# Optimization experiments

Measured on AMD Instinct MI355X. Metric: run time of the kernel, lower is better.

Reference implementation:

```python
import jax, jax.numpy as jnp
import numpy as np

FWD_W = 1.0
BWD_W = 1.0
EPS = 1e-12  # guard sqrt gradient at exact zero


def setup_inputs() -> dict:
    key = jax.random.key(0)
    k1, k2 = jax.random.split(key)
    pred = jax.random.normal(k1, (4, 8192, 3), dtype=jnp.float32)
    target = jax.random.normal(k2, (4, 8192, 3), dtype=jnp.float32)
    return {"pred": pred, "target": target}


def reference(pred, target):
    # pairwise Euclidean distances (torch.cdist, p=2): (B, N, M)
    sq = (jnp.sum(pred * pred, axis=-1)[:, :, None]
          + jnp.sum(target * target, axis=-1)[:, None, :]
          - 2.0 * jnp.einsum('bnd,bmd->bnm', pred, target))
    dist = jnp.sqrt(jnp.maximum(sq, EPS))
    forward_dist = jnp.min(dist, axis=2)   # (B, N): pred -> nearest target
    backward_dist = jnp.min(dist, axis=1)  # (B, M): target -> nearest pred
    total = FWD_W * jnp.sum(forward_dist, axis=1) + BWD_W * jnp.sum(backward_dist, axis=1)
    return jnp.mean(total)  # reduction='mean'
```

## Files before the change

### kernel.cpp

```cpp
#include <hip/hip_runtime.h>
#include <math.h>

#define BATCH   4
#define NPTS    8192
#define THREADS 256
#define NQTOT   (2 * BATCH * NPTS)
#define TSPLIT  4
#define THALF   (NPTS / TSPLIT)

typedef _Float16 h8  __attribute__((ext_vector_type(8)));
typedef float    f16v __attribute__((ext_vector_type(16)));

__global__ __launch_bounds__(THREADS)
void chamfer_transform(const float* __restrict__ pred,
                       const float* __restrict__ target,
                       h8* __restrict__ trans_il)
{
    const int p   = blockIdx.x * THREADS + threadIdx.x;
    const int arr = p >> 15;
    const int pb  = p & 32767;

    const float* src = (arr ? target : pred) + (size_t)pb * 3;
    const float x = src[0], y = src[1], z = src[2];

    const _Float16 hx = (_Float16)x;  const float lxf = x - (float)hx;
    const _Float16 hy = (_Float16)y;  const float lyf = y - (float)hy;
    const _Float16 hz = (_Float16)z;  const float lzf = z - (float)hz;
    const _Float16 lx = (_Float16)lxf, ly = (_Float16)lyf, lz = (_Float16)lzf;

    const float tx = (float)hx + (float)lx;
    const float ty = (float)hy + (float)ly;
    const float tz = (float)hz + (float)lz;
    const float tt = fmaf(tx, tx, fmaf(ty, ty, tz * tz));
    const _Float16 tth = (_Float16)tt;
    const _Float16 ttl = (_Float16)(tt - (float)tth);

    const _Float16 n2 = (_Float16)(-2.0f);
    h8 lo = { n2 * hx, n2 * hy, n2 * hz, tth,
              n2 * hx, n2 * hy, n2 * hz, ttl };
    h8 hi = { n2 * lx, n2 * ly, n2 * lz, (_Float16)0.0f,
              (_Float16)0.0f, (_Float16)0.0f, (_Float16)0.0f, (_Float16)0.0f };

    trans_il[2 * p]     = lo;
    trans_il[2 * p + 1] = hi;
}

__device__ __forceinline__ h8 make_afrag(const float* __restrict__ qp, const int hi)
{
    const float x = qp[0], y = qp[1], z = qp[2];
    const _Float16 hx = (_Float16)x; const _Float16 lx = (_Float16)(x - (float)hx);
    const _Float16 hy = (_Float16)y; const _Float16 ly = (_Float16)(y - (float)hy);
    const _Float16 hz = (_Float16)z; const _Float16 lz = (_Float16)(z - (float)hz);
    const _Float16 one  = (_Float16)1.0f;
    const _Float16 zero = (_Float16)0.0f;
    if (hi == 0) return (h8){hx, hy, hz, one, lx, ly, lz, one};
    return (h8){hx, hy, hz, zero, zero, zero, zero, zero};
}

__global__ __launch_bounds__(THREADS, 4)
void chamfer_min_kernel(const float* __restrict__ pred,
                        const float* __restrict__ target,
                        const h8* __restrict__ trans_il,
                        float* __restrict__ partial)
{
    const int tid  = threadIdx.x;
    const int lane = tid & 63;
    const int wave = tid >> 6;
    const int n    = lane & 31;
    const int hi   = lane >> 5;

    const int bid = blockIdx.x;
    const int ts  = bid & 3;
    const int qg  = (bid >> 2) & 31;
    const int b   = (bid >> 7) & 3;
    const int dir = bid >> 9;

    const int  qtbase = qg * 256 + wave * 64;
    const int  tbase  = ts * THALF;
    const int  darr   = dir ^ 1;
    const float* qraw = ((dir == 0) ? pred : target) + (size_t)b * NPTS * 3;

    const h8 afrag0 = make_afrag(qraw + (size_t)(qtbase + n) * 3, hi);
    const h8 afrag1 = make_afrag(qraw + (size_t)(qtbase + 32 + n) * 3, hi);

    float mn0[16], mn1[16];
    #pragma unroll
    for (int i = 0; i < 16; ++i) { mn0[i] = 3.0e38f; mn1[i] = 3.0e38f; }

    const size_t gbase = (size_t)(darr * 4 + b) * NPTS + tbase;
    const h8* bp = trans_il + 2 * (gbase + n) + hi;
    const f16v zc = {};

    #pragma unroll 2
    for (int tp = 0; tp < THALF / 64; ++tp) {
        const h8 b0 = bp[tp * 128];
        const h8 b1 = bp[tp * 128 + 64];

        const f16v d00 = __builtin_amdgcn_mfma_f32_32x32x16_f16(afrag0, b0, zc, 0, 0, 0);
        const f16v d01 = __builtin_amdgcn_mfma_f32_32x32x16_f16(afrag0, b1, zc, 0, 0, 0);
        #pragma unroll
        for (int i = 0; i < 16; ++i)
            mn0[i] = fminf(fminf(d00[i], d01[i]), mn0[i]);

        const f16v d10 = __builtin_amdgcn_mfma_f32_32x32x16_f16(afrag1, b0, zc, 0, 0, 0);
        const f16v d11 = __builtin_amdgcn_mfma_f32_32x32x16_f16(afrag1, b1, zc, 0, 0, 0);
        #pragma unroll
        for (int i = 0; i < 16; ++i)
            mn1[i] = fminf(fminf(d10[i], d11[i]), mn1[i]);
    }

    #pragma unroll
    for (int mask = 1; mask <= 16; mask <<= 1) {
        #pragma unroll
        for (int i = 0; i < 16; ++i) {
            mn0[i] = fminf(mn0[i], __shfl_xor(mn0[i], mask, 64));
            mn1[i] = fminf(mn1[i], __shfl_xor(mn1[i], mask, 64));
        }
    }

    if (n == 0) {
        float* dst = partial + (size_t)ts * NQTOT
                   + (size_t)(dir * 4 + b) * NPTS + qtbase;
        #pragma unroll
        for (int i = 0; i < 16; ++i) {
            const int row = (i & 3) + 8 * (i >> 2) + 4 * hi;
            dst[row]      = mn0[i];
            dst[32 + row] = mn1[i];
        }
    }
}

__global__ __launch_bounds__(THREADS)
void chamfer_reduce1(const float* __restrict__ partial,
                     const float* __restrict__ pred,
                     const float* __restrict__ target,
                     float* __restrict__ bsum)
{
    const int tid = threadIdx.x;
    const int i   = blockIdx.x * THREADS + tid;

    const float m01 = fminf(partial[i],                 partial[NQTOT + i]);
    const float m23 = fminf(partial[2 * NQTOT + i],     partial[3 * NQTOT + i]);
    const float m   = fminf(m01, m23);

    const int dir  = i >> 15;
    const int rest = i & 32767;
    const float* qp = ((dir == 0) ? pred : target) + (size_t)rest * 3;
    const float x = qp[0], y = qp[1], z = qp[2];
    const float qq = fmaf(x, x, fmaf(y, y, z * z));

    float acc = sqrtf(fmaxf(qq + m, 1e-12f));

    #pragma unroll
    for (int off = 32; off > 0; off >>= 1)
        acc += __shfl_down(acc, off, 64);

    __shared__ float wsum[4];
    if ((tid & 63) == 0) wsum[tid >> 6] = acc;
    __syncthreads();
    if (tid == 0) bsum[blockIdx.x] = wsum[0] + wsum[1] + wsum[2] + wsum[3];
}

__global__ __launch_bounds__(THREADS)
void chamfer_reduce2(const float* __restrict__ bsum,
                     float* __restrict__ out)
{
    const int tid = threadIdx.x;
    float v = bsum[tid];
    #pragma unroll
    for (int off = 32; off > 0; off >>= 1)
        v += __shfl_down(v, off, 64);

    __shared__ float wsum[4];
    if ((tid & 63) == 0) wsum[tid >> 6] = v;
    __syncthreads();
    if (tid == 0) out[0] = (wsum[0] + wsum[1] + wsum[2] + wsum[3]) * (1.0f / BATCH);
}

extern "C" void kernel_launch(void* const* d_in, const int* in_sizes, int n_in,
                              void* d_out, int out_size, void* d_ws, size_t ws_size,
                              hipStream_t stream)
{
    const float* pred   = (const float*)d_in[0];
    const float* target = (const float*)d_in[1];
    float* out          = (float*)d_out;

    h8*    trans_il = (h8*)d_ws;
    float* partial  = (float*)((char*)d_ws + (size_t)131072 * 16);
    float* bsum     = partial + (size_t)TSPLIT * NQTOT;

    chamfer_transform<<<NQTOT / THREADS, THREADS, 0, stream>>>(
        pred, target, trans_il);

    chamfer_min_kernel<<<2 * BATCH * 32 * TSPLIT, THREADS, 0, stream>>>(
        pred, target, trans_il, partial);

    chamfer_reduce1<<<NQTOT / THREADS, THREADS, 0, stream>>>(
        partial, pred, target, bsum);

    chamfer_reduce2<<<1, THREADS, 0, stream>>>(bsum, out);
}
```

Measured before the change: 83.45 us.

## Split target range across waves in-block and fuse reduce1 into min kernel

```diff
diff --git a/kernel.cpp b/kernel.cpp
--- a/kernel.cpp
+++ b/kernel.cpp
@@ -5,8 +5,7 @@
 #define NPTS    8192
 #define THREADS 256
 #define NQTOT   (2 * BATCH * NPTS)
-#define TSPLIT  4
-#define THALF   (NPTS / TSPLIT)
+#define TPW     2048
 
 typedef _Float16 h8  __attribute__((ext_vector_type(8)));
 typedef float    f16v __attribute__((ext_vector_type(16)));
@@ -57,12 +56,14 @@
     return (h8){hx, hy, hz, zero, zero, zero, zero, zero};
 }
 
-__global__ __launch_bounds__(THREADS, 4)
+__global__ __launch_bounds__(THREADS, 2)
 void chamfer_min_kernel(const float* __restrict__ pred,
                         const float* __restrict__ target,
                         const h8* __restrict__ trans_il,
-                        float* __restrict__ partial)
+                        float* __restrict__ bsum)
 {
+    __shared__ float lmn[2][4][2][16];
+
     const int tid  = threadIdx.x;
     const int lane = tid & 63;
     const int wave = tid >> 6;
@@ -70,13 +71,11 @@
     const int hi   = lane >> 5;
 
     const int bid = blockIdx.x;
-    const int ts  = bid & 3;
-    const int qg  = (bid >> 2) & 31;
+    const int qt  = bid & 127;
     const int b   = (bid >> 7) & 3;
     const int dir = bid >> 9;
 
-    const int  qtbase = qg * 256 + wave * 64;
-    const int  tbase  = ts * THALF;
+    const int  qtbase = qt * 64;
     const int  darr   = dir ^ 1;
     const float* qraw = ((dir == 0) ? pred : target) + (size_t)b * NPTS * 3;
 
@@ -87,12 +86,12 @@
     #pragma unroll
     for (int i = 0; i < 16; ++i) { mn0[i] = 3.0e38f; mn1[i] = 3.0e38f; }
 
-    const size_t gbase = (size_t)(darr * 4 + b) * NPTS + tbase;
+    const size_t gbase = (size_t)(darr * 4 + b) * NPTS + (size_t)wave * TPW;
     const h8* bp = trans_il + 2 * (gbase + n) + hi;
     const f16v zc = {};
 
-    #pragma unroll 2
-    for (int tp = 0; tp < THALF / 64; ++tp) {
+    #pragma unroll 4
+    for (int tp = 0; tp < TPW / 64; ++tp) {
         const h8 b0 = bp[tp * 128];
         const h8 b1 = bp[tp * 128 + 64];
 
@@ -119,46 +118,32 @@
     }
 
     if (n == 0) {
-        float* dst = partial + (size_t)ts * NQTOT
-                   + (size_t)(dir * 4 + b) * NPTS + qtbase;
         #pragma unroll
         for (int i = 0; i < 16; ++i) {
-            const int row = (i & 3) + 8 * (i >> 2) + 4 * hi;
-            dst[row]      = mn0[i];
-            dst[32 + row] = mn1[i];
+            lmn[0][wave][hi][i] = mn0[i];
+            lmn[1][wave][hi][i] = mn1[i];
         }
     }
-}
+    __syncthreads();
 
-__global__ __launch_bounds__(THREADS)
-void chamfer_reduce1(const float* __restrict__ partial,
-                     const float* __restrict__ pred,
-                     const float* __restrict__ target,
-                     float* __restrict__ bsum)
-{
-    const int tid = threadIdx.x;
-    const int i   = blockIdx.x * THREADS + tid;
+    if (wave == 0) {
+        const int set = lane & 1;
+        const int h2  = (lane >> 1) & 1;
+        const int i   = lane >> 2;
+        const float m = fminf(fminf(lmn[set][0][h2][i], lmn[set][1][h2][i]),
+                              fminf(lmn[set][2][h2][i], lmn[set][3][h2][i]));
+        const int r = (i & 3) + 8 * (i >> 2) + 4 * h2;
+        const int q = qtbase + 32 * set + r;
+        const float* qp = qraw + (size_t)q * 3;
+        const float x = qp[0], y = qp[1], z = qp[2];
+        const float qq = fmaf(x, x, fmaf(y, y, z * z));
+        float acc = sqrtf(fmaxf(qq + m, 1e-12f));
 
-    const float m01 = fminf(partial[i],                 partial[NQTOT + i]);
-    const float m23 = fminf(partial[2 * NQTOT + i],     partial[3 * NQTOT + i]);
-    const float m   = fminf(m01, m23);
-
-    const int dir  = i >> 15;
-    const int rest = i & 32767;
-    const float* qp = ((dir == 0) ? pred : target) + (size_t)rest * 3;
-    const float x = qp[0], y = qp[1], z = qp[2];
-    const float qq = fmaf(x, x, fmaf(y, y, z * z));
-
-    float acc = sqrtf(fmaxf(qq + m, 1e-12f));
-
-    #pragma unroll
-    for (int off = 32; off > 0; off >>= 1)
-        acc += __shfl_down(acc, off, 64);
-
-    __shared__ float wsum[4];
-    if ((tid & 63) == 0) wsum[tid >> 6] = acc;
-    __syncthreads();
-    if (tid == 0) bsum[blockIdx.x] = wsum[0] + wsum[1] + wsum[2] + wsum[3];
+        #pragma unroll
+        for (int off = 32; off > 0; off >>= 1)
+            acc += __shfl_down(acc, off, 64);
+        if (lane == 0) bsum[bid] = acc;
+    }
 }
 
 __global__ __launch_bounds__(THREADS)
@@ -166,7 +151,7 @@
                      float* __restrict__ out)
 {
     const int tid = threadIdx.x;
-    float v = bsum[tid];
+    float v = bsum[tid] + bsum[256 + tid] + bsum[512 + tid] + bsum[768 + tid];
     #pragma unroll
     for (int off = 32; off > 0; off >>= 1)
         v += __shfl_down(v, off, 64);
@@ -186,17 +171,13 @@
     float* out          = (float*)d_out;
 
     h8*    trans_il = (h8*)d_ws;
-    float* partial  = (float*)((char*)d_ws + (size_t)131072 * 16);
-    float* bsum     = partial + (size_t)TSPLIT * NQTOT;
+    float* bsum     = (float*)((char*)d_ws + (size_t)131072 * 16);
 
     chamfer_transform<<<NQTOT / THREADS, THREADS, 0, stream>>>(
         pred, target, trans_il);
 
-    chamfer_min_kernel<<<2 * BATCH * 32 * TSPLIT, THREADS, 0, stream>>>(
-        pred, target, trans_il, partial);
-
-    chamfer_reduce1<<<NQTOT / THREADS, THREADS, 0, stream>>>(
-        partial, pred, target, bsum);
+    chamfer_min_kernel<<<2 * BATCH * 128, THREADS, 0, stream>>>(
+        pred, target, trans_il, bsum);
 
     chamfer_reduce2<<<1, THREADS, 0, stream>>>(bsum, out);
 }
```

After: 82.00 us. Within noise of the previous version (-1.7%).
